# Kernel optimization log

Measured on AMD Instinct MI355X. Metric: run time of the kernel, lower is better.

The kernel has to match this reference:

```python
import jax, jax.numpy as jnp
import numpy as np

DIM = 1024
HEADS = 16
DIM_HEAD = 64
INNER = HEADS * DIM_HEAD  # 1024
MLP = 4096
NQ = 16384
NW = 1024
LN_EPS = 1e-5
L2_EPS = 1e-12


def setup_inputs() -> dict:
    key = jax.random.key(0)
    ks = jax.random.split(key, 12)
    s = 0.02
    return {
        "queries": jax.random.normal(ks[0], (NQ, DIM), jnp.float32),
        "prototypes": jax.random.normal(ks[1], (NW, DIM), jnp.float32),
        "ln1_w": 1.0 + s * jax.random.normal(ks[2], (DIM,), jnp.float32),
        "ln1_b": s * jax.random.normal(ks[3], (DIM,), jnp.float32),
        "wq": s * jax.random.normal(ks[4], (DIM, INNER), jnp.float32),
        "wk": s * jax.random.normal(ks[5], (DIM, INNER), jnp.float32),
        "wv": s * jax.random.normal(ks[6], (DIM, INNER), jnp.float32),
        "wo": s * jax.random.normal(ks[7], (INNER, DIM), jnp.float32),
        "bo": jnp.zeros((DIM,), jnp.float32),
        "ln2_w": 1.0 + s * jax.random.normal(ks[8], (DIM,), jnp.float32),
        "ln2_b": s * jax.random.normal(ks[9], (DIM,), jnp.float32),
        "w1": s * jax.random.normal(ks[10], (DIM, MLP), jnp.float32),
        "b1": jnp.zeros((MLP,), jnp.float32),
        "w2": s * jax.random.normal(ks[11], (MLP, DIM), jnp.float32),
        "b2": jnp.zeros((DIM,), jnp.float32),
    }


def _layernorm(x, w, b):
    mu = jnp.mean(x, axis=-1, keepdims=True)
    var = jnp.mean(jnp.square(x - mu), axis=-1, keepdims=True)
    return (x - mu) * jax.lax.rsqrt(var + LN_EPS) * w + b


def _l2norm(x):
    n = jnp.sqrt(jnp.sum(jnp.square(x), axis=-1, keepdims=True))
    return x / jnp.maximum(n, L2_EPS)


def reference(queries, prototypes, ln1_w, ln1_b, wq, wk, wv, wo, bo,
              ln2_w, ln2_b, w1, b1, w2, b2):
    residual = queries
    qn = _layernorm(queries, ln1_w, ln1_b)
    pn = _layernorm(prototypes, ln1_w, ln1_b)
    # projections -> (h, q, d) / (h, n, d)
    q = (qn @ wq).reshape(NQ, HEADS, DIM_HEAD).transpose(1, 0, 2)
    k = (pn @ wk).reshape(NW, HEADS, DIM_HEAD).transpose(1, 0, 2)
    v = (pn @ wv).reshape(NW, HEADS, DIM_HEAD).transpose(1, 0, 2)
    attn = jnp.einsum('hqd,hnd->hqn', _l2norm(q), _l2norm(k))  # cosine, no softmax
    out = jnp.einsum('hqn,hnd->hqd', attn, v)
    out = out.transpose(1, 0, 2).reshape(NQ, INNER)
    out = out @ wo + bo + residual
    residual2 = out
    h = _layernorm(out, ln2_w, ln2_b)
    h = jax.nn.gelu(h @ w1 + b1, approximate=False) @ w2 + b2
    return h + residual2
```

## Files before the change

kernel.cpp:

```cpp
#include <hip/hip_runtime.h>
#include <hip/hip_bf16.h>

typedef _Float16 f16;
typedef __attribute__((ext_vector_type(8))) _Float16 f16x8;
typedef __attribute__((ext_vector_type(4))) _Float16 f16x4;
typedef __attribute__((ext_vector_type(4))) float f32x4;

#define DIM 1024
#define HEADS 16
#define DHEAD 64
#define MLPD 4096
#define NQ 16384
#define NW 1024
#define MCHUNK 32

#define WAITV(n) asm volatile("s_waitcnt vmcnt(" #n ")" ::: "memory")
#define WAITL0 asm volatile("s_waitcnt lgkmcnt(0)" ::: "memory")

__device__ __forceinline__ void glds16(const f16* g, f16* l) {
  __builtin_amdgcn_global_load_lds(
      (const __attribute__((address_space(1))) void*)g,
      (__attribute__((address_space(3))) void*)l, 16, 0, 0);
}

__global__ __launch_bounds__(256) void ln_f16_k(
    const float* __restrict__ X, const float* __restrict__ w,
    const float* __restrict__ b, f16* __restrict__ O) {
  const int row = blockIdx.x;
  const int t = threadIdx.x;
  const float4 v = ((const float4*)(X + (long)row * DIM))[t];
  float s = v.x + v.y + v.z + v.w;
  float s2 = v.x * v.x + v.y * v.y + v.z * v.z + v.w * v.w;
#pragma unroll
  for (int m = 1; m < 64; m <<= 1) {
    s += __shfl_xor(s, m);
    s2 += __shfl_xor(s2, m);
  }
  __shared__ float ps[4], ps2[4];
  const int lane = t & 63, wid = t >> 6;
  if (lane == 0) { ps[wid] = s; ps2[wid] = s2; }
  __syncthreads();
  s = ps[0] + ps[1] + ps[2] + ps[3];
  s2 = ps2[0] + ps2[1] + ps2[2] + ps2[3];
  const float mu = s * (1.0f / DIM);
  const float inv = rsqrtf(s2 * (1.0f / DIM) - mu * mu + 1e-5f);
  const float4 wv = ((const float4*)w)[t];
  const float4 bv = ((const float4*)b)[t];
  f16x4 o;
  o[0] = (f16)((v.x - mu) * inv * wv.x + bv.x);
  o[1] = (f16)((v.y - mu) * inv * wv.y + bv.y);
  o[2] = (f16)((v.z - mu) * inv * wv.z + bv.z);
  o[3] = (f16)((v.w - mu) * inv * wv.w + bv.w);
  *(f16x4*)(O + (long)row * DIM + t * 4) = o;
}

__global__ __launch_bounds__(256) void tcast_k(const float* __restrict__ X,
                                               f16* __restrict__ O, int R, int C) {
  __shared__ float tile[32][33];
  const int c0 = blockIdx.x * 32, r0 = blockIdx.y * 32;
  const int tx = threadIdx.x, ty = threadIdx.y;
#pragma unroll
  for (int j = 0; j < 4; ++j)
    tile[ty + j * 8][tx] = X[(long)(r0 + ty + j * 8) * C + c0 + tx];
  __syncthreads();
#pragma unroll
  for (int j = 0; j < 4; ++j)
    O[(long)(c0 + ty + j * 8) * R + r0 + tx] = (f16)tile[tx][ty + j * 8];
}

__global__ __launch_bounds__(256) void calc_m_part_k(const f16* __restrict__ kh,
                                                     const f16* __restrict__ v,
                                                     float* __restrict__ Mp) {
  const int h = blockIdx.x, ch = blockIdx.y;
  const int t = threadIdx.x;
  const int d1 = t >> 2;
  const int d2b = (t & 3) * 16;
  float acc[16] = {};
  const int n0 = ch * (NW / MCHUNK);
#pragma unroll 4
  for (int n = n0; n < n0 + NW / MCHUNK; ++n) {
    const float kv = (float)kh[(long)n * DIM + h * DHEAD + d1];
    const f16x8* vp = (const f16x8*)&v[(long)n * DIM + h * DHEAD + d2b];
    const f16x8 v0 = vp[0], v1 = vp[1];
#pragma unroll
    for (int j = 0; j < 8; ++j) acc[j] += kv * (float)v0[j];
#pragma unroll
    for (int j = 0; j < 8; ++j) acc[8 + j] += kv * (float)v1[j];
  }
  float* o = &Mp[((long)(h * MCHUNK + ch)) * 4096 + d1 * 64 + d2b];
#pragma unroll
  for (int j = 0; j < 16; ++j) o[j] = acc[j];
}

__global__ __launch_bounds__(256) void calc_m_reduce_k(const float* __restrict__ Mp,
                                                       float* __restrict__ Mo) {
  const int h = blockIdx.x;
  const int t = threadIdx.x;
#pragma unroll
  for (int e = t; e < 4096; e += 256) {
    float s = 0.f;
#pragma unroll
    for (int c = 0; c < MCHUNK; ++c)
      s += Mp[((long)(h * MCHUNK + c)) * 4096 + e];
    Mo[h * 4096 + e] = s;
  }
}

__global__ __launch_bounds__(256) void calc_wefft_k(const float* __restrict__ M,
                                                    const float* __restrict__ wo,
                                                    f16* __restrict__ Wt) {
  const int h = blockIdx.x, jt = blockIdx.y;
  const int t = threadIdx.x;
  const int jl = t & 63;
  const int il0 = (t >> 6) * 16;
  const int j = jt * 64 + jl;
  float acc[16] = {};
  for (int d = 0; d < DHEAD; ++d) {
    const float w = wo[(long)(h * DHEAD + d) * DIM + j];
    const float* mrow = &M[h * 4096 + il0 * 64 + d];
#pragma unroll
    for (int r = 0; r < 16; ++r) acc[r] += mrow[r * 64] * w;
  }
#pragma unroll
  for (int r = 0; r < 16; ++r)
    Wt[(long)j * DIM + h * DHEAD + il0 + r] = (f16)acc[r];
}

enum {
  EPI_F16 = 0,
  EPI_L2N = 1,
  EPI_BIAS_RES = 2,
  EPI_GELU = 3
};

template <int EPI>
__global__ __launch_bounds__(512, 2) void gemm256(
    const f16* __restrict__ A, const f16* __restrict__ Bt, int M, int N, int K,
    const float* __restrict__ bias, const float* resid, void* out) {
  __shared__ __align__(16) f16 lds[65536];

  const int tid = threadIdx.x;
  const int lane = tid & 63;
  const int wid = tid >> 6;
  const int wm = wid >> 2;
  const int wn = wid & 3;
  const int l15 = lane & 15;

  int bm, bn;
  {
    const int total = gridDim.x * gridDim.y;
    const int orig = blockIdx.y * gridDim.x + blockIdx.x;
    int swz = orig;
    if ((total & 7) == 0) swz = (orig & 7) * (total >> 3) + (orig >> 3);
    bm = swz % gridDim.x;
    bn = swz / gridDim.x;
  }

  const int scol8 = (((tid & 3) ^ ((tid >> 3) & 3))) * 8;
  const f16* aSrc = A + (long)(bm * 256 + (tid >> 2)) * K + scol8;
  const f16* bSrc = Bt + (long)(bn * 256 + (tid >> 2)) * K + scol8;
  const long hK = (long)128 * K;
  const int tid8 = tid * 8;

  const int rslot8 = (((lane >> 4) ^ ((l15 >> 1) & 3))) * 8;
  const int aRdBase = (wm * 128 + l15) * 32 + rslot8;
  const int bRdBase = 16384 + (wn * 64 + l15) * 32 + rslot8;

  f32x4 acc[8][4] = {};
  const int NT = K >> 6;

  glds16(aSrc, &lds[tid8]);
  glds16(aSrc + hK, &lds[4096 + tid8]);
  glds16(bSrc, &lds[16384 + tid8]);
  glds16(bSrc + hK, &lds[16384 + 4096 + tid8]);
  glds16(aSrc + 32, &lds[8192 + tid8]);
  glds16(aSrc + hK + 32, &lds[8192 + 4096 + tid8]);
  glds16(bSrc + 32, &lds[24576 + tid8]);
  glds16(bSrc + hK + 32, &lds[24576 + 4096 + tid8]);
  glds16(aSrc + 64, &lds[32768 + tid8]);
  glds16(aSrc + hK + 64, &lds[32768 + 4096 + tid8]);
  glds16(bSrc + 64, &lds[32768 + 16384 + tid8]);
  glds16(bSrc + hK + 64, &lds[32768 + 16384 + 4096 + tid8]);
  WAITV(8);
  __builtin_amdgcn_s_barrier();

#define PHASE_CORE(KS, MH, LOADB)                                        \
  {                                                                      \
    const f16* Ap = L + (KS)*8192 + aRdBase + (MH)*2048;                 \
    a[0] = *(const f16x8*)(Ap);                                          \
    a[1] = *(const f16x8*)(Ap + 512);                                    \
    a[2] = *(const f16x8*)(Ap + 1024);                                   \
    a[3] = *(const f16x8*)(Ap + 1536);                                   \
    if (LOADB) {                                                         \
      const f16* Bp = L + (KS)*8192 + bRdBase;                           \
      b[0] = *(const f16x8*)(Bp);                                        \
      b[1] = *(const f16x8*)(Bp + 512);                                  \
      b[2] = *(const f16x8*)(Bp + 1024);                                 \
      b[3] = *(const f16x8*)(Bp + 1536);                                 \
    }                                                                    \
    __builtin_amdgcn_s_barrier();                                        \
    WAITL0;                                                              \
    __builtin_amdgcn_sched_barrier(0);                                   \
    __builtin_amdgcn_s_setprio(1);                                       \
    _Pragma("unroll") for (int j = 0; j < 4; ++j)                        \
        _Pragma("unroll") for (int nj = 0; nj < 4; ++nj)                 \
            acc[(MH)*4 + j][nj] = __builtin_amdgcn_mfma_f32_16x16x32_f16(\
                a[j], b[nj], acc[(MH)*4 + j][nj], 0, 0, 0);              \
    __builtin_amdgcn_s_setprio(0);                                       \
  }

  for (int g = 0; g < NT; ++g) {
    f16* L = &lds[(g & 1) * 32768];
    f16* Lo = &lds[((g & 1) ^ 1) * 32768];
    const long ko1 = (long)(g + 1) * 64;
    const long ko2 = (long)(g + 2) * 64;
    const bool s1 = (g + 1) < NT, s2 = (g + 2) < NT;
    f16x8 a[4], b[4];

    if (s1) {
      glds16(aSrc + ko1 + 32, Lo + 8192 + tid8);
      glds16(aSrc + hK + ko1 + 32, Lo + 8192 + 4096 + tid8);
    }
    PHASE_CORE(0, 0, 1);
    __builtin_amdgcn_s_barrier();

    if (s1) {
      glds16(bSrc + ko1 + 32, Lo + 24576 + tid8);
      glds16(bSrc + hK + ko1 + 32, Lo + 24576 + 4096 + tid8);
    }
    PHASE_CORE(0, 1, 0);
    if (s1) { WAITV(8); } else { WAITV(0); }
    __builtin_amdgcn_s_barrier();

    if (s2) {
      glds16(aSrc + ko2, L + tid8);
      glds16(aSrc + hK + ko2, L + 4096 + tid8);
    }
    PHASE_CORE(1, 0, 1);
    __builtin_amdgcn_s_barrier();

    if (s2) {
      glds16(bSrc + ko2, L + 16384 + tid8);
      glds16(bSrc + hK + ko2, L + 16384 + 4096 + tid8);
    }
    PHASE_CORE(1, 1, 0);
    if (s2) { WAITV(8); } else if (s1) { WAITV(4); }
    __builtin_amdgcn_s_barrier();
  }
#undef PHASE_CORE

  const int r0 = bm * 256 + wm * 128;
  const int c0 = bn * 256 + wn * 64;
  const int lr = (lane >> 4) * 4;
  const int lc = l15;

#pragma unroll
  for (int mi = 0; mi < 8; ++mi) {
#pragma unroll
    for (int i = 0; i < 4; ++i) {
      const long r = r0 + mi * 16 + lr + i;
      if (EPI == EPI_L2N) {
        float ss = 0.f;
#pragma unroll
        for (int nj = 0; nj < 4; ++nj) {
          const float x = acc[mi][nj][i];
          ss += x * x;
        }
        ss += __shfl_xor(ss, 1);
        ss += __shfl_xor(ss, 2);
        ss += __shfl_xor(ss, 4);
        ss += __shfl_xor(ss, 8);
        const float inv = 1.0f / fmaxf(sqrtf(ss), 1e-12f);
#pragma unroll
        for (int nj = 0; nj < 4; ++nj)
          ((f16*)out)[r * N + c0 + nj * 16 + lc] = (f16)(acc[mi][nj][i] * inv);
      } else if (EPI == EPI_F16) {
#pragma unroll
        for (int nj = 0; nj < 4; ++nj)
          ((f16*)out)[r * N + c0 + nj * 16 + lc] = (f16)acc[mi][nj][i];
      } else if (EPI == EPI_BIAS_RES) {
#pragma unroll
        for (int nj = 0; nj < 4; ++nj) {
          const long c = c0 + nj * 16 + lc;
          ((float*)out)[r * N + c] = acc[mi][nj][i] + bias[c] + resid[r * N + c];
        }
      } else {
#pragma unroll
        for (int nj = 0; nj < 4; ++nj) {
          const long c = c0 + nj * 16 + lc;
          const float x = acc[mi][nj][i] + bias[c];
          ((f16*)out)[r * N + c] =
              (f16)(0.5f * x * (1.0f + erff(x * 0.70710678118654752f)));
        }
      }
    }
  }
}

extern "C" void kernel_launch(void* const* d_in, const int* in_sizes, int n_in,
                              void* d_out, int out_size, void* d_ws, size_t ws_size,
                              hipStream_t stream) {
  (void)in_sizes; (void)n_in; (void)out_size;
  const float* queries = (const float*)d_in[0];
  const float* prototypes = (const float*)d_in[1];
  const float* ln1_w = (const float*)d_in[2];
  const float* ln1_b = (const float*)d_in[3];
  const float* wq = (const float*)d_in[4];
  const float* wk = (const float*)d_in[5];
  const float* wv = (const float*)d_in[6];
  const float* wo = (const float*)d_in[7];
  const float* bo = (const float*)d_in[8];
  const float* ln2_w = (const float*)d_in[9];
  const float* ln2_b = (const float*)d_in[10];
  const float* w1 = (const float*)d_in[11];
  const float* b1 = (const float*)d_in[12];
  const float* w2 = (const float*)d_in[13];
  const float* b2 = (const float*)d_in[14];

  char* ws = (char*)d_ws;
  const size_t MB = 1024ull * 1024ull;
  if (ws_size < 176ull * MB) return;

  f16* QN = (f16*)(ws + 0);
  f16* QHAT = (f16*)(ws + 32 * MB);
  f16* PN = (f16*)(ws + 64 * MB);
  f16* WQT = (f16*)(ws + 66 * MB);
  f16* WKT = (f16*)(ws + 68 * MB);
  f16* WVT = (f16*)(ws + 70 * MB);
  f16* KHAT = (f16*)(ws + 72 * MB);
  f16* VBF = (f16*)(ws + 74 * MB);
  float* Mbuf = (float*)(ws + 76 * MB);
  f16* WEFFT = (f16*)(ws + 77 * MB);
  float* Mpart = (float*)(ws + 0);
  f16* G = (f16*)(ws + 0);
  f16* HBF = (f16*)(ws + 128 * MB);
  f16* W1T = (f16*)(ws + 160 * MB);
  f16* W2T = (f16*)(ws + 168 * MB);
  float* RES2 = (float*)d_out;

  ln_f16_k<<<NQ, 256, 0, stream>>>(queries, ln1_w, ln1_b, QN);
  ln_f16_k<<<NW, 256, 0, stream>>>(prototypes, ln1_w, ln1_b, PN);
  tcast_k<<<dim3(32, 32), dim3(32, 8), 0, stream>>>(wq, WQT, DIM, DIM);
  tcast_k<<<dim3(32, 32), dim3(32, 8), 0, stream>>>(wk, WKT, DIM, DIM);
  tcast_k<<<dim3(32, 32), dim3(32, 8), 0, stream>>>(wv, WVT, DIM, DIM);
  tcast_k<<<dim3(128, 32), dim3(32, 8), 0, stream>>>(w1, W1T, DIM, MLPD);
  tcast_k<<<dim3(32, 128), dim3(32, 8), 0, stream>>>(w2, W2T, MLPD, DIM);

  gemm256<EPI_L2N><<<dim3(NQ / 256, DIM / 256), 512, 0, stream>>>(
      QN, WQT, NQ, DIM, DIM, nullptr, nullptr, QHAT);
  gemm256<EPI_L2N><<<dim3(NW / 256, DIM / 256), 512, 0, stream>>>(
      PN, WKT, NW, DIM, DIM, nullptr, nullptr, KHAT);
  gemm256<EPI_F16><<<dim3(NW / 256, DIM / 256), 512, 0, stream>>>(
      PN, WVT, NW, DIM, DIM, nullptr, nullptr, VBF);

  calc_m_part_k<<<dim3(HEADS, MCHUNK), 256, 0, stream>>>(KHAT, VBF, Mpart);
  calc_m_reduce_k<<<HEADS, 256, 0, stream>>>(Mpart, Mbuf);
  calc_wefft_k<<<dim3(HEADS, 16), 256, 0, stream>>>(Mbuf, wo, WEFFT);

  gemm256<EPI_BIAS_RES><<<dim3(NQ / 256, DIM / 256), 512, 0, stream>>>(
      QHAT, WEFFT, NQ, DIM, DIM, bo, queries, RES2);

  ln_f16_k<<<NQ, 256, 0, stream>>>(RES2, ln2_w, ln2_b, HBF);

  gemm256<EPI_GELU><<<dim3(NQ / 256, MLPD / 256), 512, 0, stream>>>(
      HBF, W1T, NQ, MLPD, DIM, b1, nullptr, G);
  gemm256<EPI_BIAS_RES><<<dim3(NQ / 256, DIM / 256), 512, 0, stream>>>(
      G, W2T, NQ, DIM, MLPD, b2, RES2, (float*)d_out);
}
```

Baseline: 693.1 us.

## Store residual in fp16, use tanh GELU, split MLP into row chunks, new tile swizzle

The attention output residual is now stored as fp16 in the workspace instead of fp32 in the output buffer, and a new layernorm kernel reads fp16 input. GELU switches from erf to a tanh approximation built on exp. The MLP runs in two 8192-row chunks so the intermediate activation stays smaller, which may keep it more cache-resident. The block swizzle is also changed to slab along M. The aim is to cut memory traffic and transcendental cost, at the price of rounding the residual to fp16, an approximate GELU, and smaller grids per launch.

```diff
diff --git a/kernel.cpp b/kernel.cpp
--- a/kernel.cpp
+++ b/kernel.cpp
@@ -54,6 +54,39 @@
   *(f16x4*)(O + (long)row * DIM + t * 4) = o;
 }
 
+__global__ __launch_bounds__(256) void ln_f16in_k(
+    const f16* __restrict__ X, const float* __restrict__ w,
+    const float* __restrict__ b, f16* __restrict__ O) {
+  const int row = blockIdx.x;
+  const int t = threadIdx.x;
+  const f16x4 hv = *(const f16x4*)(X + (long)row * DIM + t * 4);
+  const float x0 = (float)hv[0], x1 = (float)hv[1], x2 = (float)hv[2],
+              x3 = (float)hv[3];
+  float s = x0 + x1 + x2 + x3;
+  float s2 = x0 * x0 + x1 * x1 + x2 * x2 + x3 * x3;
+#pragma unroll
+  for (int m = 1; m < 64; m <<= 1) {
+    s += __shfl_xor(s, m);
+    s2 += __shfl_xor(s2, m);
+  }
+  __shared__ float ps[4], ps2[4];
+  const int lane = t & 63, wid = t >> 6;
+  if (lane == 0) { ps[wid] = s; ps2[wid] = s2; }
+  __syncthreads();
+  s = ps[0] + ps[1] + ps[2] + ps[3];
+  s2 = ps2[0] + ps2[1] + ps2[2] + ps2[3];
+  const float mu = s * (1.0f / DIM);
+  const float inv = rsqrtf(s2 * (1.0f / DIM) - mu * mu + 1e-5f);
+  const float4 wv = ((const float4*)w)[t];
+  const float4 bv = ((const float4*)b)[t];
+  f16x4 o;
+  o[0] = (f16)((x0 - mu) * inv * wv.x + bv.x);
+  o[1] = (f16)((x1 - mu) * inv * wv.y + bv.y);
+  o[2] = (f16)((x2 - mu) * inv * wv.z + bv.z);
+  o[3] = (f16)((x3 - mu) * inv * wv.w + bv.w);
+  *(f16x4*)(O + (long)row * DIM + t * 4) = o;
+}
+
 __global__ __launch_bounds__(256) void tcast_k(const float* __restrict__ X,
                                                f16* __restrict__ O, int R, int C) {
   __shared__ float tile[32][33];
@@ -129,14 +162,15 @@
 enum {
   EPI_F16 = 0,
   EPI_L2N = 1,
-  EPI_BIAS_RES = 2,
-  EPI_GELU = 3
+  EPI_ATTN = 2,
+  EPI_GELU = 3,
+  EPI_OUT = 4
 };
 
 template <int EPI>
 __global__ __launch_bounds__(512, 2) void gemm256(
     const f16* __restrict__ A, const f16* __restrict__ Bt, int M, int N, int K,
-    const float* __restrict__ bias, const float* resid, void* out) {
+    const float* __restrict__ bias, const void* resid, void* out) {
   __shared__ __align__(16) f16 lds[65536];
 
   const int tid = threadIdx.x;
@@ -148,12 +182,17 @@
 
   int bm, bn;
   {
-    const int total = gridDim.x * gridDim.y;
     const int orig = blockIdx.y * gridDim.x + blockIdx.x;
-    int swz = orig;
-    if ((total & 7) == 0) swz = (orig & 7) * (total >> 3) + (orig >> 3);
-    bm = swz % gridDim.x;
-    bn = swz / gridDim.x;
+    if ((gridDim.x & 7) == 0) {
+      const int slab = orig & 7;
+      const int idx = orig >> 3;
+      const int sm = gridDim.x >> 3;
+      bm = slab * sm + idx % sm;
+      bn = idx / sm;
+    } else {
+      bm = blockIdx.x;
+      bn = blockIdx.y;
+    }
   }
 
   const int scol8 = (((tid & 3) ^ ((tid >> 3) & 3))) * 8;
@@ -278,19 +317,29 @@
 #pragma unroll
         for (int nj = 0; nj < 4; ++nj)
           ((f16*)out)[r * N + c0 + nj * 16 + lc] = (f16)acc[mi][nj][i];
-      } else if (EPI == EPI_BIAS_RES) {
+      } else if (EPI == EPI_ATTN) {
 #pragma unroll
         for (int nj = 0; nj < 4; ++nj) {
           const long c = c0 + nj * 16 + lc;
-          ((float*)out)[r * N + c] = acc[mi][nj][i] + bias[c] + resid[r * N + c];
+          ((f16*)out)[r * N + c] =
+              (f16)(acc[mi][nj][i] + bias[c] + ((const float*)resid)[r * N + c]);
         }
-      } else {
+      } else if (EPI == EPI_GELU) {
 #pragma unroll
         for (int nj = 0; nj < 4; ++nj) {
           const long c = c0 + nj * 16 + lc;
           const float x = acc[mi][nj][i] + bias[c];
-          ((f16*)out)[r * N + c] =
-              (f16)(0.5f * x * (1.0f + erff(x * 0.70710678118654752f)));
+          const float u = 0.7978845608028654f * (x + 0.044715f * x * x * x);
+          const float z = __expf(fminf(-2.0f * u, 88.0f));
+          const float th = (1.0f - z) / (1.0f + z);
+          ((f16*)out)[r * N + c] = (f16)(0.5f * x * (1.0f + th));
+        }
+      } else {
+#pragma unroll
+        for (int nj = 0; nj < 4; ++nj) {
+          const long c = c0 + nj * 16 + lc;
+          ((float*)out)[r * N + c] =
+              acc[mi][nj][i] + bias[c] + (float)((const f16*)resid)[r * N + c];
         }
       }
     }
@@ -319,7 +368,7 @@
 
   char* ws = (char*)d_ws;
   const size_t MB = 1024ull * 1024ull;
-  if (ws_size < 176ull * MB) return;
+  if (ws_size < 160ull * MB) return;
 
   f16* QN = (f16*)(ws + 0);
   f16* QHAT = (f16*)(ws + 32 * MB);
@@ -333,10 +382,10 @@
   f16* WEFFT = (f16*)(ws + 77 * MB);
   float* Mpart = (float*)(ws + 0);
   f16* G = (f16*)(ws + 0);
-  f16* HBF = (f16*)(ws + 128 * MB);
-  f16* W1T = (f16*)(ws + 160 * MB);
-  f16* W2T = (f16*)(ws + 168 * MB);
-  float* RES2 = (float*)d_out;
+  f16* RES2 = (f16*)(ws + 80 * MB);
+  f16* HBF = (f16*)(ws + 112 * MB);
+  f16* W1T = (f16*)(ws + 144 * MB);
+  f16* W2T = (f16*)(ws + 152 * MB);
 
   ln_f16_k<<<NQ, 256, 0, stream>>>(queries, ln1_w, ln1_b, QN);
   ln_f16_k<<<NW, 256, 0, stream>>>(prototypes, ln1_w, ln1_b, PN);
@@ -357,13 +406,17 @@
   calc_m_reduce_k<<<HEADS, 256, 0, stream>>>(Mpart, Mbuf);
   calc_wefft_k<<<dim3(HEADS, 16), 256, 0, stream>>>(Mbuf, wo, WEFFT);
 
-  gemm256<EPI_BIAS_RES><<<dim3(NQ / 256, DIM / 256), 512, 0, stream>>>(
+  gemm256<EPI_ATTN><<<dim3(NQ / 256, DIM / 256), 512, 0, stream>>>(
       QHAT, WEFFT, NQ, DIM, DIM, bo, queries, RES2);
 
-  ln_f16_k<<<NQ, 256, 0, stream>>>(RES2, ln2_w, ln2_b, HBF);
-
-  gemm256<EPI_GELU><<<dim3(NQ / 256, MLPD / 256), 512, 0, stream>>>(
-      HBF, W1T, NQ, MLPD, DIM, b1, nullptr, G);
-  gemm256<EPI_BIAS_RES><<<dim3(NQ / 256, DIM / 256), 512, 0, stream>>>(
-      G, W2T, NQ, DIM, MLPD, b2, RES2, (float*)d_out);
-}
+  ln_f16in_k<<<NQ, 256, 0, stream>>>(RES2, ln2_w, ln2_b, HBF);
+
+  for (int c = 0; c < 2; ++c) {
+    const long ro = (long)c * 8192;
+    gemm256<EPI_GELU><<<dim3(32, MLPD / 256), 512, 0, stream>>>(
+        HBF + ro * DIM, W1T, 8192, MLPD, DIM, b1, nullptr, G);
+    gemm256<EPI_OUT><<<dim3(32, DIM / 256), 512, 0, stream>>>(
+        G, W2T, 8192, DIM, MLPD, b2, RES2 + ro * DIM,
+        (float*)d_out + ro * DIM);
+  }
+}
```

After: 684.3 us. Within noise of the previous version (-1.3%).
